# Optimization experiments

Measured on AMD Instinct MI355X. Metric: run time of the kernel, lower is better.

## Reference

```python
import jax, jax.numpy as jnp
import numpy as np

N_NODES = 100000
N_EDGES = 1600000
D_IN = 64
D_HID = 64
D_OUT = 10
N_GRAPHS = 512


def setup_inputs() -> dict:
    key = jax.random.key(0)
    ks = jax.random.split(key, 12)
    x = jax.random.normal(ks[0], (N_NODES, D_IN), dtype=jnp.float32)
    edge_index = jax.random.randint(ks[1], (2, N_EDGES), 0, N_NODES, dtype=jnp.int64)
    batch = jnp.sort(jax.random.randint(ks[2], (N_NODES,), 0, N_GRAPHS, dtype=jnp.int64))
    def lin_w(k, fan_in, fan_out):
        s = 1.0 / np.sqrt(fan_in)
        return jax.random.uniform(k, (fan_in, fan_out), jnp.float32, -s, s)
    # Per PyG GraphConv: lin_rel (with bias) on aggregated neighbors, lin_root (no bias) on self.
    params = {
        'W_rel1': lin_w(ks[3], D_IN, D_HID),  'b_rel1': jnp.zeros((D_HID,), jnp.float32), 'W_root1': lin_w(ks[4], D_IN, D_HID),
        'W_rel2': lin_w(ks[5], D_HID, D_HID), 'b_rel2': jnp.zeros((D_HID,), jnp.float32), 'W_root2': lin_w(ks[6], D_HID, D_HID),
        'W_rel3': lin_w(ks[7], D_HID, D_HID), 'b_rel3': jnp.zeros((D_HID,), jnp.float32), 'W_root3': lin_w(ks[8], D_HID, D_HID),
        'W_lin': lin_w(ks[9], D_HID, D_OUT),  'b_lin': jnp.zeros((D_OUT,), jnp.float32),
    }
    return {'x': x, 'edge_index': edge_index, 'batch': batch, **params}


def _graph_conv(x, src, dst, W_rel, b_rel, W_root):
    # sum-aggregate messages x[src] at dst nodes, then two linear maps
    agg = jax.ops.segment_sum(x[src], dst, num_segments=N_NODES)
    return agg @ W_rel + b_rel + x @ W_root


def reference(x, edge_index, batch,
              W_rel1, b_rel1, W_root1,
              W_rel2, b_rel2, W_root2,
              W_rel3, b_rel3, W_root3,
              W_lin, b_lin):
    src, dst = edge_index[0], edge_index[1]
    h = jax.nn.relu(_graph_conv(x, src, dst, W_rel1, b_rel1, W_root1))
    h = jax.nn.relu(_graph_conv(h, src, dst, W_rel2, b_rel2, W_root2))
    h = _graph_conv(h, src, dst, W_rel3, b_rel3, W_root3)
    # global_mean_pool over graph ids
    sums = jax.ops.segment_sum(h, batch, num_segments=N_GRAPHS)
    counts = jax.ops.segment_sum(jnp.ones((h.shape[0], 1), h.dtype), batch, num_segments=N_GRAPHS)
    pooled = sums / jnp.maximum(counts, 1.0)
    return pooled @ W_lin + b_lin
```

## Files before the change

### kernel.cpp

```cpp
#include <hip/hip_runtime.h>

#define NN 100000
#define NE 1600000
#define DF 64
#define NG 512
#define DOUT 10
#define NPART 8
#define PSZ 12500

typedef unsigned short u16;
typedef unsigned int   u32;
typedef __attribute__((ext_vector_type(8))) short short8;
typedef __attribute__((ext_vector_type(4))) float f32x4;

__device__ __forceinline__ float bflo(u32 u) { union { u32 u; float f; } x; x.u = u << 16;        return x.f; }
__device__ __forceinline__ float bfhi(u32 u) { union { u32 u; float f; } x; x.u = u & 0xFFFF0000u; return x.f; }
__device__ __forceinline__ u32 f2bf(float f) {
    union { float f; u32 u; } x; x.f = f;
    return (x.u + 0x7FFFu + ((x.u >> 16) & 1u)) >> 16;
}
__device__ __forceinline__ u32 pk(float lo, float hi) { return f2bf(lo) | (f2bf(hi) << 16); }

__global__ __launch_bounds__(256) void k_cursor_init(int* __restrict__ cursor) {
    int n = blockIdx.x * 256 + threadIdx.x;
    if (n < NN) cursor[n] = n << 6;
}

__global__ __launch_bounds__(256) void k_fill(const int* __restrict__ src,
                                              const int* __restrict__ dst,
                                              int* __restrict__ cursor,
                                              int* __restrict__ csr) {
    int part = blockIdx.x & (NPART - 1);
    int e = (blockIdx.x >> 3) * 256 + threadIdx.x;
    if (e >= NE) return;
    int d = dst[e];
    if (d / PSZ != part) return;
    int pos = atomicAdd(&cursor[d], 1);
    if (pos < (d << 6) + 64) csr[pos] = src[e];
}

__global__ __launch_bounds__(256) void k_cvt(const float* __restrict__ x,
                                             u16* __restrict__ xb) {
    int i = blockIdx.x * 256 + threadIdx.x;
    if (i >= NN * 8) return;
    const float4* p = (const float4*)x + (size_t)i * 2;
    float4 a = p[0], b = p[1];
    uint4 o;
    o.x = pk(a.x, a.y); o.y = pk(a.z, a.w);
    o.z = pk(b.x, b.y); o.w = pk(b.z, b.w);
    ((uint4*)xb)[i] = o;
}

__global__ __launch_bounds__(256) void k_wprep(const float* __restrict__ Wrel,
                                               const float* __restrict__ Wroot,
                                               u16* __restrict__ whi,
                                               u16* __restrict__ wlo) {
    int i = blockIdx.x * 256 + threadIdx.x;
    if (i >= 8192) return;
    int j  = i & 7;
    int l  = (i >> 3) & 63;
    int kh = (i >> 9) & 1;
    int ct = (i >> 10) & 3;
    int m  = i >> 12;
    int k = kh * 32 + ((l >> 4) << 3) + j;
    int o = ct * 16 + (l & 15);
    const float* W = m ? Wroot : Wrel;
    float v = W[k * 64 + o];
    u32 hi = f2bf(v);
    union { u32 u; float f; } hf; hf.u = hi << 16;
    u32 lo = f2bf(v - hf.f);
    whi[i] = (u16)hi;
    wlo[i] = (u16)lo;
}

__global__ __launch_bounds__(256) void k_gather(const u16* __restrict__ hb,
                                                const int* __restrict__ csr,
                                                const int* __restrict__ cursor,
                                                u16* __restrict__ aggb) {
    int tid = blockIdx.x * 256 + threadIdx.x;
    int n = tid >> 3;
    if (n >= NN) return;
    int c8 = (tid & 7) << 3;
    int beg = n << 6;
    int cnt = cursor[n] - beg; if (cnt > 64) cnt = 64;
    const int* lst = csr + beg;
    float a0=0,a1=0,a2=0,a3=0,a4=0,a5=0,a6=0,a7=0;
    int j = 0;
    for (; j + 7 < cnt; j += 8) {
        int idx[8];
#pragma unroll
        for (int q = 0; q < 8; ++q) idx[q] = lst[j + q];
        uint4 v[8];
#pragma unroll
        for (int q = 0; q < 8; ++q) v[q] = *(const uint4*)(hb + (size_t)idx[q] * DF + c8);
#pragma unroll
        for (int q = 0; q < 8; ++q) {
            a0 += bflo(v[q].x); a1 += bfhi(v[q].x);
            a2 += bflo(v[q].y); a3 += bfhi(v[q].y);
            a4 += bflo(v[q].z); a5 += bfhi(v[q].z);
            a6 += bflo(v[q].w); a7 += bfhi(v[q].w);
        }
    }
    for (; j < cnt; ++j) {
        uint4 v = *(const uint4*)(hb + (size_t)lst[j] * DF + c8);
        a0 += bflo(v.x); a1 += bfhi(v.x);
        a2 += bflo(v.y); a3 += bfhi(v.y);
        a4 += bflo(v.z); a5 += bfhi(v.z);
        a6 += bflo(v.w); a7 += bfhi(v.w);
    }
    uint4 o;
    o.x = pk(a0,a1); o.y = pk(a2,a3); o.z = pk(a4,a5); o.w = pk(a6,a7);
    *(uint4*)(aggb + (size_t)n * DF + c8) = o;
}

template <bool RELU>
__global__ __launch_bounds__(256) void k_lin_mfma(const u16* __restrict__ aggb,
                                                  const u16* __restrict__ hb,
                                                  const u16* __restrict__ whi,
                                                  const u16* __restrict__ wlo,
                                                  const float* __restrict__ brel,
                                                  u16* __restrict__ outb) {
    const int t = threadIdx.x;
    const int w = t >> 6, l = t & 63;
    const int lh = l & 15, kg = l >> 4;
    const int node = blockIdx.x * 64 + w * 16 + lh;
    const bool ok = node < NN;

    short8 bA0 = 0, bA1 = 0, bH0 = 0, bH1 = 0;
    if (ok) {
        const u16* pa = aggb + (size_t)node * DF + kg * 8;
        const u16* ph = hb   + (size_t)node * DF + kg * 8;
        bA0 = *(const short8*)pa;
        bA1 = *(const short8*)(pa + 32);
        bH0 = *(const short8*)ph;
        bH1 = *(const short8*)(ph + 32);
    }

#pragma unroll
    for (int ct = 0; ct < 4; ++ct) {
        const float4 bb = *(const float4*)(brel + ct * 16 + kg * 4);
        f32x4 acc = { bb.x, bb.y, bb.z, bb.w };
        const int lo8 = l * 8;
        short8 a0 = *(const short8*)(whi + ((0*4 + ct)*2 + 0)*512 + lo8);
        short8 a1 = *(const short8*)(whi + ((0*4 + ct)*2 + 1)*512 + lo8);
        short8 a2 = *(const short8*)(wlo + ((0*4 + ct)*2 + 0)*512 + lo8);
        short8 a3 = *(const short8*)(wlo + ((0*4 + ct)*2 + 1)*512 + lo8);
        short8 a4 = *(const short8*)(whi + ((1*4 + ct)*2 + 0)*512 + lo8);
        short8 a5 = *(const short8*)(whi + ((1*4 + ct)*2 + 1)*512 + lo8);
        short8 a6 = *(const short8*)(wlo + ((1*4 + ct)*2 + 0)*512 + lo8);
        short8 a7 = *(const short8*)(wlo + ((1*4 + ct)*2 + 1)*512 + lo8);
        acc = __builtin_amdgcn_mfma_f32_16x16x32_bf16(a0, bA0, acc, 0, 0, 0);
        acc = __builtin_amdgcn_mfma_f32_16x16x32_bf16(a1, bA1, acc, 0, 0, 0);
        acc = __builtin_amdgcn_mfma_f32_16x16x32_bf16(a2, bA0, acc, 0, 0, 0);
        acc = __builtin_amdgcn_mfma_f32_16x16x32_bf16(a3, bA1, acc, 0, 0, 0);
        acc = __builtin_amdgcn_mfma_f32_16x16x32_bf16(a4, bH0, acc, 0, 0, 0);
        acc = __builtin_amdgcn_mfma_f32_16x16x32_bf16(a5, bH1, acc, 0, 0, 0);
        acc = __builtin_amdgcn_mfma_f32_16x16x32_bf16(a6, bH0, acc, 0, 0, 0);
        acc = __builtin_amdgcn_mfma_f32_16x16x32_bf16(a7, bH1, acc, 0, 0, 0);
        if (RELU) {
            acc[0] = fmaxf(acc[0], 0.f); acc[1] = fmaxf(acc[1], 0.f);
            acc[2] = fmaxf(acc[2], 0.f); acc[3] = fmaxf(acc[3], 0.f);
        }
        if (ok) {
            uint2 o;
            o.x = pk(acc[0], acc[1]);
            o.y = pk(acc[2], acc[3]);
            *(uint2*)(outb + (size_t)node * DF + ct * 16 + kg * 4) = o;
        }
    }
}

__global__ __launch_bounds__(256) void k_gstart(const int* __restrict__ batch,
                                                int* __restrict__ gstart) {
    int g = blockIdx.x * 256 + threadIdx.x;
    if (g > NG) return;
    int lo = 0, hi = NN;
    while (lo < hi) {
        int mid = (lo + hi) >> 1;
        if (batch[mid] < g) lo = mid + 1; else hi = mid;
    }
    gstart[g] = lo;
}

__global__ __launch_bounds__(256) void k_pool(const u16* __restrict__ hb,
                                              const int* __restrict__ gstart,
                                              float* __restrict__ pooled) {
    int g = blockIdx.x;
    int beg = gstart[g], end = gstart[g + 1];
    int lane = threadIdx.x & 63, wv = threadIdx.x >> 6;
    float acc = 0.f;
    for (int n = beg + wv; n < end; n += 4)
        acc += bflo((u32)hb[(size_t)n * DF + lane]);
    __shared__ float red[4][DF];
    red[wv][lane] = acc;
    __syncthreads();
    if (wv == 0) {
        float s = red[0][lane] + red[1][lane] + red[2][lane] + red[3][lane];
        pooled[(size_t)g * DF + lane] = s / fmaxf((float)(end - beg), 1.0f);
    }
}

__global__ __launch_bounds__(256) void k_head(const float* __restrict__ pooled,
                                              const float* __restrict__ Wlin,
                                              const float* __restrict__ blin,
                                              float* __restrict__ out) {
    int tid = blockIdx.x * 256 + threadIdx.x;
    if (tid >= NG * DOUT) return;
    int g = tid / DOUT;
    int j = tid - g * DOUT;
    float acc = blin[j];
#pragma unroll
    for (int k = 0; k < DF; ++k)
        acc += pooled[(size_t)g * DF + k] * Wlin[k * DOUT + j];
    out[(size_t)g * DOUT + j] = acc;
}

extern "C" void kernel_launch(void* const* d_in, const int* in_sizes, int n_in,
                              void* d_out, int out_size, void* d_ws, size_t ws_size,
                              hipStream_t stream) {
    (void)in_sizes; (void)n_in; (void)out_size; (void)ws_size;
    const float* x      = (const float*)d_in[0];
    const int*   edges  = (const int*)d_in[1];
    const int*   batch  = (const int*)d_in[2];
    const float* Wrel1  = (const float*)d_in[3];
    const float* brel1  = (const float*)d_in[4];
    const float* Wroot1 = (const float*)d_in[5];
    const float* Wrel2  = (const float*)d_in[6];
    const float* brel2  = (const float*)d_in[7];
    const float* Wroot2 = (const float*)d_in[8];
    const float* Wrel3  = (const float*)d_in[9];
    const float* brel3  = (const float*)d_in[10];
    const float* Wroot3 = (const float*)d_in[11];
    const float* Wlin   = (const float*)d_in[12];
    const float* blin   = (const float*)d_in[13];
    float* out = (float*)d_out;

    const int* src = edges;
    const int* dst = edges + NE;

    char* w = (char*)d_ws;
    u16* xb     = (u16*)(w);
    u16* hA     = (u16*)(w + 12800000);
    u16* hB     = (u16*)(w + 25600000);
    u16* aggb   = (u16*)(w + 38400000);
    float* pooled = (float*)(w + 51200000);
    int* csr    = (int*)(w + 51331072);
    int* cursor = (int*)(w + 76931072);
    int* gstart = (int*)(w + 77331072);
    u16* whiB   = (u16*)(w + 77333504);
    u16* wloB   = (u16*)(w + 77333504 + 3*8192*2);

    dim3 blk(256);

    k_cursor_init<<<(NN + 255) / 256, blk, 0, stream>>>(cursor);
    k_fill<<<((NE + 255) / 256) * NPART, blk, 0, stream>>>(src, dst, cursor, csr);
    k_cvt<<<(NN * 8 + 255) / 256, blk, 0, stream>>>(x, xb);
    k_gstart<<<3, blk, 0, stream>>>(batch, gstart);
    k_wprep<<<32, blk, 0, stream>>>(Wrel1, Wroot1, whiB + 0*8192, wloB + 0*8192);
    k_wprep<<<32, blk, 0, stream>>>(Wrel2, Wroot2, whiB + 1*8192, wloB + 1*8192);
    k_wprep<<<32, blk, 0, stream>>>(Wrel3, Wroot3, whiB + 2*8192, wloB + 2*8192);

    dim3 gGat((NN * 8 + 255) / 256);
    dim3 gLin((NN + 63) / 64);

    k_gather<<<gGat, blk, 0, stream>>>(xb, csr, cursor, aggb);
    k_lin_mfma<true><<<gLin, blk, 0, stream>>>(aggb, xb, whiB + 0*8192, wloB + 0*8192, brel1, hA);
    k_gather<<<gGat, blk, 0, stream>>>(hA, csr, cursor, aggb);
    k_lin_mfma<true><<<gLin, blk, 0, stream>>>(aggb, hA, whiB + 1*8192, wloB + 1*8192, brel2, hB);
    k_gather<<<gGat, blk, 0, stream>>>(hB, csr, cursor, aggb);
    k_lin_mfma<false><<<gLin, blk, 0, stream>>>(aggb, hB, whiB + 2*8192, wloB + 2*8192, brel3, hA);

    k_pool<<<NG, blk, 0, stream>>>(hA, gstart, pooled);
    k_head<<<(NG * DOUT + 255) / 256, blk, 0, stream>>>(pooled, Wlin, blin, out);
}
```

Baseline: 355.7 us.

## Fuse neighbor gather into MFMA linear kernel via shared-memory aggregate tile

Merges the gather and the MFMA linear kernels so each block aggregates 32 nodes into a shared-memory tile and then runs the bf16 MFMA transform on it. This drops the aggb round trip through global memory and three kernel launches per forward. Each wave now covers two of the four output column tiles, and blocks shrink to 32 nodes. The edge fill also switches to nontemporal loads for src and dst.

```diff
diff --git a/kernel.cpp b/kernel.cpp
--- a/kernel.cpp
+++ b/kernel.cpp
@@ -33,10 +33,10 @@
     int part = blockIdx.x & (NPART - 1);
     int e = (blockIdx.x >> 3) * 256 + threadIdx.x;
     if (e >= NE) return;
-    int d = dst[e];
+    int d = __builtin_nontemporal_load(&dst[e]);
     if (d / PSZ != part) return;
     int pos = atomicAdd(&cursor[d], 1);
-    if (pos < (d << 6) + 64) csr[pos] = src[e];
+    if (pos < (d << 6) + 64) csr[pos] = __builtin_nontemporal_load(&src[e]);
 }
 
 __global__ __launch_bounds__(256) void k_cvt(const float* __restrict__ x,
@@ -73,71 +73,69 @@
     wlo[i] = (u16)lo;
 }
 
-__global__ __launch_bounds__(256) void k_gather(const u16* __restrict__ hb,
-                                                const int* __restrict__ csr,
-                                                const int* __restrict__ cursor,
-                                                u16* __restrict__ aggb) {
-    int tid = blockIdx.x * 256 + threadIdx.x;
-    int n = tid >> 3;
-    if (n >= NN) return;
-    int c8 = (tid & 7) << 3;
-    int beg = n << 6;
-    int cnt = cursor[n] - beg; if (cnt > 64) cnt = 64;
-    const int* lst = csr + beg;
-    float a0=0,a1=0,a2=0,a3=0,a4=0,a5=0,a6=0,a7=0;
-    int j = 0;
-    for (; j + 7 < cnt; j += 8) {
-        int idx[8];
-#pragma unroll
-        for (int q = 0; q < 8; ++q) idx[q] = lst[j + q];
-        uint4 v[8];
-#pragma unroll
-        for (int q = 0; q < 8; ++q) v[q] = *(const uint4*)(hb + (size_t)idx[q] * DF + c8);
-#pragma unroll
-        for (int q = 0; q < 8; ++q) {
-            a0 += bflo(v[q].x); a1 += bfhi(v[q].x);
-            a2 += bflo(v[q].y); a3 += bfhi(v[q].y);
-            a4 += bflo(v[q].z); a5 += bfhi(v[q].z);
-            a6 += bflo(v[q].w); a7 += bfhi(v[q].w);
+template <bool RELU>
+__global__ __launch_bounds__(256) void k_glin(const u16* __restrict__ hb,
+                                              const int* __restrict__ csr,
+                                              const int* __restrict__ cursor,
+                                              const u16* __restrict__ whi,
+                                              const u16* __restrict__ wlo,
+                                              const float* __restrict__ brel,
+                                              u16* __restrict__ outb) {
+    __shared__ u16 sAgg[32][72];
+    const int t = threadIdx.x;
+    const int node0 = blockIdx.x * 32;
+
+    {
+        int n = node0 + (t >> 3);
+        int c8 = (t & 7) << 3;
+        int beg = n << 6;
+        int cnt = cursor[n] - beg; if (cnt > 64) cnt = 64;
+        const int* lst = csr + beg;
+        float a0=0,a1=0,a2=0,a3=0,a4=0,a5=0,a6=0,a7=0;
+        int j = 0;
+        for (; j + 7 < cnt; j += 8) {
+            int idx[8];
+#pragma unroll
+            for (int q = 0; q < 8; ++q) idx[q] = lst[j + q];
+            uint4 v[8];
+#pragma unroll
+            for (int q = 0; q < 8; ++q) v[q] = *(const uint4*)(hb + (size_t)idx[q] * DF + c8);
+#pragma unroll
+            for (int q = 0; q < 8; ++q) {
+                a0 += bflo(v[q].x); a1 += bfhi(v[q].x);
+                a2 += bflo(v[q].y); a3 += bfhi(v[q].y);
+                a4 += bflo(v[q].z); a5 += bfhi(v[q].z);
+                a6 += bflo(v[q].w); a7 += bfhi(v[q].w);
+            }
         }
-    }
-    for (; j < cnt; ++j) {
-        uint4 v = *(const uint4*)(hb + (size_t)lst[j] * DF + c8);
-        a0 += bflo(v.x); a1 += bfhi(v.x);
-        a2 += bflo(v.y); a3 += bfhi(v.y);
-        a4 += bflo(v.z); a5 += bfhi(v.z);
-        a6 += bflo(v.w); a7 += bfhi(v.w);
-    }
-    uint4 o;
-    o.x = pk(a0,a1); o.y = pk(a2,a3); o.z = pk(a4,a5); o.w = pk(a6,a7);
-    *(uint4*)(aggb + (size_t)n * DF + c8) = o;
-}
-
-template <bool RELU>
-__global__ __launch_bounds__(256) void k_lin_mfma(const u16* __restrict__ aggb,
-                                                  const u16* __restrict__ hb,
-                                                  const u16* __restrict__ whi,
-                                                  const u16* __restrict__ wlo,
-                                                  const float* __restrict__ brel,
-                                                  u16* __restrict__ outb) {
-    const int t = threadIdx.x;
+        for (; j < cnt; ++j) {
+            uint4 v = *(const uint4*)(hb + (size_t)lst[j] * DF + c8);
+            a0 += bflo(v.x); a1 += bfhi(v.x);
+            a2 += bflo(v.y); a3 += bfhi(v.y);
+            a4 += bflo(v.z); a5 += bfhi(v.z);
+            a6 += bflo(v.w); a7 += bfhi(v.w);
+        }
+        uint4 o;
+        o.x = pk(a0,a1); o.y = pk(a2,a3); o.z = pk(a4,a5); o.w = pk(a6,a7);
+        *(uint4*)&sAgg[t >> 3][c8] = o;
+    }
+    __syncthreads();
+
     const int w = t >> 6, l = t & 63;
     const int lh = l & 15, kg = l >> 4;
-    const int node = blockIdx.x * 64 + w * 16 + lh;
-    const bool ok = node < NN;
-
-    short8 bA0 = 0, bA1 = 0, bH0 = 0, bH1 = 0;
-    if (ok) {
-        const u16* pa = aggb + (size_t)node * DF + kg * 8;
-        const u16* ph = hb   + (size_t)node * DF + kg * 8;
-        bA0 = *(const short8*)pa;
-        bA1 = *(const short8*)(pa + 32);
-        bH0 = *(const short8*)ph;
-        bH1 = *(const short8*)(ph + 32);
-    }
-
-#pragma unroll
-    for (int ct = 0; ct < 4; ++ct) {
+    const int ng = w >> 1;
+    const int lnode = ng * 16 + lh;
+    const int node = node0 + lnode;
+
+    short8 bA0 = *(const short8*)&sAgg[lnode][kg * 8];
+    short8 bA1 = *(const short8*)&sAgg[lnode][32 + kg * 8];
+    const u16* ph = hb + (size_t)node * DF + kg * 8;
+    short8 bH0 = *(const short8*)ph;
+    short8 bH1 = *(const short8*)(ph + 32);
+
+#pragma unroll
+    for (int cc = 0; cc < 2; ++cc) {
+        const int ct = (w & 1) * 2 + cc;
         const float4 bb = *(const float4*)(brel + ct * 16 + kg * 4);
         f32x4 acc = { bb.x, bb.y, bb.z, bb.w };
         const int lo8 = l * 8;
@@ -161,12 +159,10 @@
             acc[0] = fmaxf(acc[0], 0.f); acc[1] = fmaxf(acc[1], 0.f);
             acc[2] = fmaxf(acc[2], 0.f); acc[3] = fmaxf(acc[3], 0.f);
         }
-        if (ok) {
-            uint2 o;
-            o.x = pk(acc[0], acc[1]);
-            o.y = pk(acc[2], acc[3]);
-            *(uint2*)(outb + (size_t)node * DF + ct * 16 + kg * 4) = o;
-        }
+        uint2 o;
+        o.x = pk(acc[0], acc[1]);
+        o.y = pk(acc[2], acc[3]);
+        *(uint2*)(outb + (size_t)node * DF + ct * 16 + kg * 4) = o;
     }
 }
 
@@ -242,13 +238,12 @@
     u16* xb     = (u16*)(w);
     u16* hA     = (u16*)(w + 12800000);
     u16* hB     = (u16*)(w + 25600000);
-    u16* aggb   = (u16*)(w + 38400000);
-    float* pooled = (float*)(w + 51200000);
-    int* csr    = (int*)(w + 51331072);
-    int* cursor = (int*)(w + 76931072);
-    int* gstart = (int*)(w + 77331072);
-    u16* whiB   = (u16*)(w + 77333504);
-    u16* wloB   = (u16*)(w + 77333504 + 3*8192*2);
+    float* pooled = (float*)(w + 38400000);
+    int* csr    = (int*)(w + 38531072);
+    int* cursor = (int*)(w + 64131072);
+    int* gstart = (int*)(w + 64531072);
+    u16* whiB   = (u16*)(w + 64533504);
+    u16* wloB   = (u16*)(w + 64533504 + 3*8192*2);
 
     dim3 blk(256);
 
@@ -260,15 +255,11 @@
     k_wprep<<<32, blk, 0, stream>>>(Wrel2, Wroot2, whiB + 1*8192, wloB + 1*8192);
     k_wprep<<<32, blk, 0, stream>>>(Wrel3, Wroot3, whiB + 2*8192, wloB + 2*8192);
 
-    dim3 gGat((NN * 8 + 255) / 256);
-    dim3 gLin((NN + 63) / 64);
-
-    k_gather<<<gGat, blk, 0, stream>>>(xb, csr, cursor, aggb);
-    k_lin_mfma<true><<<gLin, blk, 0, stream>>>(aggb, xb, whiB + 0*8192, wloB + 0*8192, brel1, hA);
-    k_gather<<<gGat, blk, 0, stream>>>(hA, csr, cursor, aggb);
-    k_lin_mfma<true><<<gLin, blk, 0, stream>>>(aggb, hA, whiB + 1*8192, wloB + 1*8192, brel2, hB);
-    k_gather<<<gGat, blk, 0, stream>>>(hB, csr, cursor, aggb);
-    k_lin_mfma<false><<<gLin, blk, 0, stream>>>(aggb, hB, whiB + 2*8192, wloB + 2*8192, brel3, hA);
+    dim3 gGL(NN / 32);
+
+    k_glin<true><<<gGL, blk, 0, stream>>>(xb, csr, cursor, whiB + 0*8192, wloB + 0*8192, brel1, hA);
+    k_glin<true><<<gGL, blk, 0, stream>>>(hA, csr, cursor, whiB + 1*8192, wloB + 1*8192, brel2, hB);
+    k_glin<false><<<gGL, blk, 0, stream>>>(hB, csr, cursor, whiB + 2*8192, wloB + 2*8192, brel3, hA);
 
     k_pool<<<NG, blk, 0, stream>>>(hA, gstart, pooled);
     k_head<<<(NG * DOUT + 255) / 256, blk, 0, stream>>>(pooled, Wlin, blin, out);
```

After: 338.3 us. 1.05x faster.
